# Performance work log

Hardware: AMD Instinct MI355X
Metric: run time of the kernel (lower is better)

Reference implementation:

```python
import jax, jax.numpy as jnp
import numpy as np

B, S, D = 1, 1024, 1024
NH, DH, DR = 8, 128, 64
DCQ, DC = 768, 256
INTER, E, TOPK = 512, 8, 2

def rmsnorm(x, w, eps=1e-6):
    return x * jax.lax.rsqrt(jnp.mean(x * x, -1, keepdims=True) + eps) * w

def lin(x, w, b):
    return x @ w.T + b

def apply_rope(x, cos, sin):
    # x: [b, s, h, d]; cos/sin: [S, d//2]; complex rotate pairs (even, odd)
    b, s, h, d = x.shape
    xr = x.reshape(b, s, h, d // 2, 2)
    x0, x1 = xr[..., 0], xr[..., 1]
    c = cos[None, :s, None, :]
    sn = sin[None, :s, None, :]
    return jnp.stack([x0 * c - x1 * sn, x0 * sn + x1 * c], -1).reshape(b, s, h, d)

def setup_inputs():
    keys = iter(jax.random.split(jax.random.key(0), 64))
    def nrm(*shape):
        return jax.random.normal(next(keys), shape, jnp.float32) * 0.02
    theta = 1.0 / (10000.0 ** (jnp.arange(0, DR, 2, dtype=jnp.float32) / DR))
    ang = jnp.arange(S, dtype=jnp.float32)[:, None] * theta[None, :]
    return dict(
        h=jax.random.normal(next(keys), (B, S, D), jnp.float32),
        freqs_cos=jnp.cos(ang), freqs_sin=jnp.sin(ang),
        mask=jnp.triu(jnp.ones((S, S), bool), 1),
        attn_norm_w=jnp.ones(D), ffn_norm_w=jnp.ones(D),
        wq_down=nrm(DCQ, D), bq_down=jnp.zeros(DCQ), q_norm_w=jnp.ones(DCQ),
        wqc=nrm(NH * DH, DCQ), bqc=jnp.zeros(NH * DH),
        wqr=nrm(NH * DR, DCQ), bqr=jnp.zeros(NH * DR),
        wkr=nrm(DR, D), bkr=jnp.zeros(DR), kr_norm_w=jnp.ones(DR),
        wkv_down=nrm(DC, D), bkv_down=jnp.zeros(DC), kv_norm_w=jnp.ones(DC),
        wkc=nrm(NH * DH, DC), bkc=jnp.zeros(NH * DH),
        wvc=nrm(NH * DH, DC), bvc=jnp.zeros(NH * DH),
        wo=nrm(D, NH * DH), bo=jnp.zeros(D),
        sw1=nrm(INTER, D), sb1=jnp.zeros(INTER), sw2=nrm(D, INTER), sb2=jnp.zeros(D),
        sw3=nrm(INTER, D), sb3=jnp.zeros(INTER),
        ew1=nrm(E, INTER, D), eb1=jnp.zeros((E, INTER)), ew2=nrm(E, D, INTER), eb2=jnp.zeros((E, D)),
        ew3=nrm(E, INTER, D), eb3=jnp.zeros((E, INTER)),
        centroids=jax.random.normal(next(keys), (E, D), jnp.float32), biases=jnp.zeros(E),
    )

def _forward(h, freqs_cos, freqs_sin, mask, attn_norm_w, ffn_norm_w, wq_down, bq_down, q_norm_w, wqc, bqc, wqr, bqr, wkr, bkr, kr_norm_w, wkv_down, bkv_down, kv_norm_w, wkc, bkc, wvc, bvc, wo, bo, sw1, sb1, sw2, sb2, sw3, sb3, ew1, eb1, ew2, eb2, ew3, eb3, centroids, biases):
    b, s, _ = h.shape
    # --- pre-norm MLA attention ---
    x = rmsnorm(h, attn_norm_w)
    cQ = rmsnorm(lin(x, wq_down, bq_down), q_norm_w)
    qR = apply_rope(lin(cQ, wqr, bqr).reshape(b, s, NH, DR), freqs_cos, freqs_sin)
    qC = lin(cQ, wqc, bqc).reshape(b, s, NH, DH)
    q = jnp.concatenate([qC, qR], -1)                      # [b,s,NH,DH+DR]
    kR = apply_rope(rmsnorm(lin(x, wkr, bkr), kr_norm_w).reshape(b, s, 1, DR), freqs_cos, freqs_sin)
    cKV = rmsnorm(lin(x, wkv_down, bkv_down), kv_norm_w)
    kC = lin(cKV, wkc, bkc).reshape(b, s, NH, DH)
    vC = lin(cKV, wvc, bvc).reshape(b, s, NH, DH)
    k = jnp.concatenate([jnp.broadcast_to(kR, (b, s, NH, DR)), kC], -1)  # source order: [kR, kC]
    scores = jnp.einsum('bqhd,bkhd->bhqk', q, k) / jnp.sqrt(jnp.float32(DH + DR))
    scores = jnp.where(mask[None, None], jnp.finfo(scores.dtype).min, scores)
    attw = jax.nn.softmax(scores, -1)                      # dropout in eval mode = identity
    attn = jnp.einsum('bhqk,bkhd->bqhd', attw, vC).reshape(b, s, NH * DH)
    x1 = h + lin(attn, wo, bo)
    # --- pre-norm MoE FFN ---
    y = rmsnorm(x1, ffn_norm_w)
    shared = lin(jax.nn.silu(lin(y, sw1, sb1)) * lin(y, sw3, sb3), sw2, sb2)  # mean over 1 shared expert
    affinity = jax.nn.sigmoid(y @ centroids.T)             # [b,s,E]
    _, topi = jax.lax.top_k(affinity + biases, TOPK)
    gates = jax.nn.softmax(jnp.take_along_axis(affinity, topi, -1), -1)      # [b,s,TOPK]
    combine = (jax.nn.one_hot(topi, E, dtype=y.dtype) * gates[..., None]).sum(-2)  # [b,s,E]
    h1 = jax.nn.silu(jnp.einsum('bsd,eid->bsei', y, ew1) + eb1) * (jnp.einsum('bsd,eid->bsei', y, ew3) + eb3)
    out_e = jnp.einsum('bsei,edi->bsed', h1, ew2) + eb2
    routed = (out_e * combine[..., None]).sum(2)
    return x1 + shared + routed

def reference(h, freqs_cos, freqs_sin, mask, attn_norm_w, ffn_norm_w, wq_down, bq_down, q_norm_w, wqc, bqc, wqr, bqr, wkr, bkr, kr_norm_w, wkv_down, bkv_down, kv_norm_w, wkc, bkc, wvc, bvc, wo, bo, sw1, sb1, sw2, sb2, sw3, sb3, ew1, eb1, ew2, eb2, ew3, eb3, centroids, biases):
    return _forward(h, freqs_cos, freqs_sin, mask, attn_norm_w, ffn_norm_w, wq_down, bq_down, q_norm_w, wqc, bqc, wqr, bqr, wkr, bkr, kr_norm_w, wkv_down, bkv_down, kv_norm_w, wkc, bkc, wvc, bvc, wo, bo, sw1, sb1, sw2, sb2, sw3, sb3, ew1, eb1, ew2, eb2, ew3, eb3, centroids, biases)
```

## Files before the change

### kernel.cpp

```cpp
#include <hip/hip_runtime.h>

typedef unsigned short u16;
typedef __attribute__((ext_vector_type(8))) short short8;
typedef __attribute__((ext_vector_type(4))) float f32x4;

__device__ __forceinline__ float b2f(u16 u) { return __uint_as_float(((unsigned)u) << 16); }
__device__ __forceinline__ u16 f2b(float f) {
    unsigned x = __float_as_uint(f);
    return (u16)((x + 0x7fffu + ((x >> 16) & 1u)) >> 16);
}

#define GLDS16(gp, lp) __builtin_amdgcn_global_load_lds( \
    (const __attribute__((address_space(1))) void*)(gp), \
    (__attribute__((address_space(3))) void*)(lp), 16, 0, 0)

#define WAITV(N) do { \
    asm volatile("s_waitcnt vmcnt(" #N ")" ::: "memory"); \
    __builtin_amdgcn_sched_barrier(0); \
} while (0)

#define KC8_SWZ(lane) ((((lane) & 3) ^ (((lane) >> 3) & 3)) << 3)
#define RD_SWZ(fm, fq) (((fq) ^ (((fm) >> 1) & 3)) << 3)

struct Seg { const u16* W; const float* bias; void* C; int ldc; int epi; int bx0; int aidx; };
struct GArgs {
    const u16* A[2]; int lda[2]; int K[2];
    Seg seg[4]; int nseg;
    const float* res;
    float* dst2;
};

__launch_bounds__(256)
__global__ void mgemm4(GArgs ga)
{
    __shared__ u16 As[4 * 2048];
    __shared__ u16 Bs[4 * 2048];
    int bx = blockIdx.x, by = blockIdx.y;
    int si = 0;
#pragma unroll
    for (int i = 1; i < 4; i++)
        if (i < ga.nseg && bx >= ga.seg[i].bx0) si = i;
    const u16* Wp = ga.seg[si].W;
    const float* bp = ga.seg[si].bias;
    void* Cp = ga.seg[si].C;
    const int ldco = ga.seg[si].ldc;
    const int epi = ga.seg[si].epi;
    const int ai = ga.seg[si].aidx;
    const u16* Ap = ga.A[ai];
    const int lda = ga.lda[ai], K = ga.K[ai];
    const int col0 = (bx - ga.seg[si].bx0) * 64;
    const int row0 = by * 64;

    int tid = threadIdx.x;
    int lane = tid & 63, w = tid >> 6;
    int r0 = (w << 4) + (lane >> 2), kc8 = KC8_SWZ(lane);
    const u16* gA = Ap + (size_t)(row0 + r0) * lda + kc8;
    const u16* gB = Wp + (size_t)(col0 + r0) * lda + kc8;

    int fm = lane & 15, fq = lane >> 4;
    const int so = RD_SWZ(fm, fq);
    f32x4 acc[4] = {};

#define MG_STAGE(BS, KO) do { \
    GLDS16(gA + (KO), As + (BS) * 2048 + (w << 9)); \
    GLDS16(gB + (KO), Bs + (BS) * 2048 + (w << 9)); \
} while (0)

    const int nst = K >> 5;
    MG_STAGE(0, 0);
    MG_STAGE(1, 32);
    MG_STAGE(2, 64);
    int bc = 0;
    for (int t = 0; t < nst; t++) {
        if (t < nst - 2) WAITV(4);
        else if (t == nst - 2) WAITV(2);
        else WAITV(0);
        __builtin_amdgcn_s_barrier();
        if (t + 3 < nst) {
            int bs = bc + 3; if (bs >= 4) bs -= 4;
            MG_STAGE(bs, (t + 3) << 5);
        }
        short8 af = *(const short8*)(As + bc * 2048 + (w << 9) + fm * 32 + so);
        short8 bf[4];
#pragma unroll
        for (int nt = 0; nt < 4; nt++)
            bf[nt] = *(const short8*)(Bs + bc * 2048 + ((nt << 4) + fm) * 32 + so);
#pragma unroll
        for (int nt = 0; nt < 4; nt++)
            acc[nt] = __builtin_amdgcn_mfma_f32_16x16x32_bf16(af, bf[nt], acc[nt], 0, 0, 0);
        bc = (bc + 1) & 3;
    }
#undef MG_STAGE

    int rbase = row0 + (w << 4) + (fq << 2);
#pragma unroll
    for (int nt = 0; nt < 4; nt++) {
        int c = col0 + (nt << 4) + fm;
        float bcol = bp[c];
#pragma unroll
        for (int reg = 0; reg < 4; reg++) {
            int r = rbase + reg;
            float v = acc[nt][reg] + bcol;
            if (epi == 3)
                ((u16*)Cp)[(size_t)r * ldco + c] = f2b(v);
            else if (epi == 1) {
                float o = v + ga.res[(size_t)r * ldco + c];
                ((float*)Cp)[(size_t)r * ldco + c] = o;
                if (ga.dst2) ga.dst2[(size_t)r * ldco + c] = o;
            } else
                ((float*)Cp)[(size_t)r * ldco + c] = v;
        }
    }
}

__launch_bounds__(256)
__global__ void mega_glu(const u16* __restrict__ Y16,
                         const u16* __restrict__ sw1, const float* __restrict__ sb1,
                         const u16* __restrict__ sw3, const float* __restrict__ sb3,
                         const u16* __restrict__ ew1, const float* __restrict__ eb1,
                         const u16* __restrict__ ew3, const float* __restrict__ eb3,
                         u16* __restrict__ Gb,
                         const int* __restrict__ lists, const int* __restrict__ counts)
{
    __shared__ u16 As[4 * 2048];
    __shared__ u16 B1s[4 * 2048];
    __shared__ u16 B3s[4 * 2048];
    int bx = blockIdx.x, by = blockIdx.y, z = blockIdx.z;
    int col0 = bx * 64;
    int cnt = 1024; const int* list = nullptr;
    const u16 *W1p, *W3p; const float *b1p, *b3p;
    if (z == 0) {
        W1p = sw1; b1p = sb1; W3p = sw3; b3p = sb3;
    } else {
        int e = z - 1; cnt = counts[e]; list = lists + (e << 10);
        W1p = ew1 + (size_t)e * 512 * 1024; b1p = eb1 + e * 512;
        W3p = ew3 + (size_t)e * 512 * 1024; b3p = eb3 + e * 512;
    }
    int row0 = by * 64;
    if (row0 >= cnt) return;
    u16* Cp = Gb + (size_t)z * 524288;

    int tid = threadIdx.x, lane = tid & 63, w = tid >> 6;
    int r0 = (w << 4) + (lane >> 2), kc8 = KC8_SWZ(lane);
    int ar = row0 + r0;
    if (z > 0) ar = list[ar < cnt ? ar : cnt - 1];
    const u16* gA = Y16 + (size_t)ar * 1024 + kc8;
    const u16* gB1 = W1p + (size_t)(col0 + r0) * 1024 + kc8;
    const u16* gB3 = W3p + (size_t)(col0 + r0) * 1024 + kc8;

    int fm = lane & 15, fq = lane >> 4;
    const int so = RD_SWZ(fm, fq);
    f32x4 accU[4] = {}, accV[4] = {};

#define GL_STAGE(BS, KO) do { \
    GLDS16(gA + (KO),  As  + (BS) * 2048 + (w << 9)); \
    GLDS16(gB1 + (KO), B1s + (BS) * 2048 + (w << 9)); \
    GLDS16(gB3 + (KO), B3s + (BS) * 2048 + (w << 9)); \
} while (0)

    GL_STAGE(0, 0);
    GL_STAGE(1, 32);
    GL_STAGE(2, 64);
    int bc = 0;
    for (int t = 0; t < 32; t++) {
        if (t < 30) WAITV(6);
        else if (t == 30) WAITV(3);
        else WAITV(0);
        __builtin_amdgcn_s_barrier();
        if (t + 3 < 32) {
            int bs = bc + 3; if (bs >= 4) bs -= 4;
            GL_STAGE(bs, (t + 3) << 5);
        }
        short8 af = *(const short8*)(As + bc * 2048 + (w << 9) + fm * 32 + so);
#pragma unroll
        for (int nt = 0; nt < 4; nt++) {
            short8 b1 = *(const short8*)(B1s + bc * 2048 + ((nt << 4) + fm) * 32 + so);
            accU[nt] = __builtin_amdgcn_mfma_f32_16x16x32_bf16(af, b1, accU[nt], 0, 0, 0);
        }
#pragma unroll
        for (int nt = 0; nt < 4; nt++) {
            short8 b3 = *(const short8*)(B3s + bc * 2048 + ((nt << 4) + fm) * 32 + so);
            accV[nt] = __builtin_amdgcn_mfma_f32_16x16x32_bf16(af, b3, accV[nt], 0, 0, 0);
        }
        bc = (bc + 1) & 3;
    }
#undef GL_STAGE

    int rbase = row0 + (w << 4) + (fq << 2);
#pragma unroll
    for (int nt = 0; nt < 4; nt++) {
        int c = col0 + (nt << 4) + fm;
        float b1c = b1p[c], b3c = b3p[c];
#pragma unroll
        for (int reg = 0; reg < 4; reg++) {
            int r = rbase + reg;
            if (r >= cnt) continue;
            float u = b2f(f2b(accU[nt][reg] + b1c));
            float v = b2f(f2b(accV[nt][reg] + b3c));
            Cp[(size_t)r * 512 + c] = f2b(u / (1.f + __expf(-u)) * v);
        }
    }
}

__launch_bounds__(256)
__global__ void mega_down(const u16* __restrict__ Gb,
                          const u16* __restrict__ sw2, const float* __restrict__ sb2,
                          const u16* __restrict__ ew2, const float* __restrict__ eb2,
                          float* __restrict__ out,
                          const int* __restrict__ lists, const float* __restrict__ glist,
                          const int* __restrict__ counts)
{
    __shared__ u16 Gs[4 * 2048];
    __shared__ u16 Ws[4 * 2048];
    int bx = blockIdx.x, by = blockIdx.y, z = blockIdx.z;
    int cnt = 1024; const int* list = nullptr; const float* gl = nullptr;
    const u16* Wp; const float* bp;
    if (z == 0) { Wp = sw2; bp = sb2; }
    else {
        int e = z - 1;
        cnt = counts[e]; list = lists + (e << 10); gl = glist + (e << 10);
        Wp = ew2 + (size_t)e * 1024 * 512; bp = eb2 + e * 1024;
    }
    int row0 = by * 64;
    if (row0 >= cnt) return;
    const u16* Ap = Gb + (size_t)z * 524288;
    int col0 = bx * 64;

    int tid = threadIdx.x, lane = tid & 63, w = tid >> 6;
    int r0 = (w << 4) + (lane >> 2), kc8 = KC8_SWZ(lane);
    const u16* gG = Ap + (size_t)(row0 + r0) * 512 + kc8;
    const u16* gW = Wp + (size_t)(col0 + r0) * 512 + kc8;

    int fm = lane & 15, fq = lane >> 4;
    const int so = RD_SWZ(fm, fq);
    f32x4 acc[4] = {};

#define MD_STAGE(BS, KO) do { \
    GLDS16(gG + (KO), Gs + (BS) * 2048 + (w << 9)); \
    GLDS16(gW + (KO), Ws + (BS) * 2048 + (w << 9)); \
} while (0)

    MD_STAGE(0, 0);
    MD_STAGE(1, 32);
    MD_STAGE(2, 64);
    int bc = 0;
    for (int t = 0; t < 16; t++) {
        if (t < 14) WAITV(4);
        else if (t == 14) WAITV(2);
        else WAITV(0);
        __builtin_amdgcn_s_barrier();
        if (t + 3 < 16) {
            int bs = bc + 3; if (bs >= 4) bs -= 4;
            MD_STAGE(bs, (t + 3) << 5);
        }
        short8 af = *(const short8*)(Gs + bc * 2048 + (w << 9) + fm * 32 + so);
        short8 bf[4];
#pragma unroll
        for (int nt = 0; nt < 4; nt++)
            bf[nt] = *(const short8*)(Ws + bc * 2048 + ((nt << 4) + fm) * 32 + so);
#pragma unroll
        for (int nt = 0; nt < 4; nt++)
            acc[nt] = __builtin_amdgcn_mfma_f32_16x16x32_bf16(af, bf[nt], acc[nt], 0, 0, 0);
        bc = (bc + 1) & 3;
    }
#undef MD_STAGE

    int rbase = row0 + (w << 4) + (fq << 2);
#pragma unroll
    for (int nt = 0; nt < 4; nt++) {
        int c = col0 + (nt << 4) + fm;
        float bcol = bp[c];
#pragma unroll
        for (int reg = 0; reg < 4; reg++) {
            int r = rbase + reg;
            int tok; float g;
            if (z == 0) { tok = r; g = 1.f; }
            else { if (r >= cnt) continue; tok = list[r]; g = gl[r]; }
            atomicAdd(&out[(size_t)tok * 1024 + c], g * (acc[nt][reg] + bcol));
        }
    }
}

__launch_bounds__(256)
__global__ void attn_mfma(const u16* __restrict__ Qp, const u16* __restrict__ Kp,
                          const u16* __restrict__ VT, u16* __restrict__ O)
{
    const int qt = blockIdx.x, h = blockIdx.y;
    const int q0 = qt * 64;
    const int tid = threadIdx.x;
    const int lane = tid & 63, w = tid >> 6;
    const int fm = lane & 15, fq = lane >> 4;

    __shared__ u16 Ks[2 * 12288];
    __shared__ u16 Vs[4 * 4096];
    __shared__ u16 Ps[4 * 2048];

    const u16* qrow = Qp + ((size_t)h * 1024 + q0 + w * 16 + fm) * 192;
    short8 qf[6];
#pragma unroll
    for (int c = 0; c < 6; c++)
        qf[c] = *(const short8*)(qrow + c * 32 + fq * 8);

    const u16* Kb = Kp + (size_t)h * 1024 * 192;
    const u16* Vb = VT + (size_t)h * 128 * 1024;

    float m_i[4], l_i[4];
#pragma unroll
    for (int r = 0; r < 4; r++) { m_i[r] = -1e30f; l_i[r] = 0.f; }
    f32x4 accO[8] = {};
    const float scale = 0.07216878364870323f;
    const int nkt = (qt >> 1) + 1;
    const int rbase = w * 16 + fq * 4;

    for (int kt = 0; kt < nkt; ++kt) {
        const int kt0 = kt * 128;
#pragma unroll
        for (int half = 0; half < 2; half++) {
            const int o = kt0 + half * 64;
#pragma unroll
            for (int i = 0; i < 6; i++) {
                int idx = w + 4 * i;
                int c = idx >> 2, k4 = idx & 3;
                const u16* g = Kb + (size_t)(o + k4 * 16 + (lane >> 2)) * 192 + c * 32 + (lane & 3) * 8;
                GLDS16(g, Ks + half * 12288 + c * 2048 + k4 * 512 + lane * 8);
            }
#pragma unroll
            for (int i = 0; i < 4; i++) {
                int idx = w + 4 * i;
                int kc = idx >> 3, k8 = idx & 7;
                const u16* g = Vb + (size_t)(k8 * 16 + (lane >> 2)) * 1024 + o + kc * 32 + (lane & 3) * 8;
                GLDS16(g, Vs + (half * 2 + kc) * 4096 + k8 * 512 + lane * 8);
            }
        }
        __syncthreads();
        f32x4 sacc[8];
#pragma unroll
        for (int nt = 0; nt < 8; nt++) {
            sacc[nt] = (f32x4){0.f, 0.f, 0.f, 0.f};
#pragma unroll
            for (int c = 0; c < 6; c++) {
                short8 kf = *(const short8*)(Ks + (nt >> 2) * 12288 + c * 2048 + ((nt & 3) * 16 + fm) * 32 + fq * 8);
                sacc[nt] = __builtin_amdgcn_mfma_f32_16x16x32_bf16(qf[c], kf, sacc[nt], 0, 0, 0);
            }
        }
        float pv[8][4], rmax[4];
#pragma unroll
        for (int reg = 0; reg < 4; reg++) {
            int q = q0 + rbase + reg;
            float mx = -1e30f;
#pragma unroll
            for (int nt = 0; nt < 8; nt++) {
                int gk = kt0 + nt * 16 + fm;
                float s = sacc[nt][reg] * scale;
                if (gk > q) s = -1e30f;
                pv[nt][reg] = s;
                mx = fmaxf(mx, s);
            }
            rmax[reg] = mx;
        }
#pragma unroll
        for (int m = 1; m < 16; m <<= 1)
#pragma unroll
            for (int reg = 0; reg < 4; reg++)
                rmax[reg] = fmaxf(rmax[reg], __shfl_xor(rmax[reg], m));
        float alpha[4], rsum[4];
#pragma unroll
        for (int reg = 0; reg < 4; reg++) {
            float mn = fmaxf(m_i[reg], rmax[reg]);
            alpha[reg] = __expf(m_i[reg] - mn);
            m_i[reg] = mn;
            float s = 0.f;
#pragma unroll
            for (int nt = 0; nt < 8; nt++) {
                float p = __expf(pv[nt][reg] - mn);
                pv[nt][reg] = p;
                s += p;
            }
            rsum[reg] = s;
        }
#pragma unroll
        for (int m = 1; m < 16; m <<= 1)
#pragma unroll
            for (int reg = 0; reg < 4; reg++)
                rsum[reg] += __shfl_xor(rsum[reg], m);
#pragma unroll
        for (int reg = 0; reg < 4; reg++)
            l_i[reg] = l_i[reg] * alpha[reg] + rsum[reg];
#pragma unroll
        for (int nt = 0; nt < 8; nt++)
#pragma unroll
            for (int reg = 0; reg < 4; reg++)
                Ps[w * 2048 + (nt >> 1) * 512 + (fq * 4 + reg) * 32 + (nt & 1) * 16 + fm]
                    = f2b(pv[nt][reg]);
#pragma unroll
        for (int n2 = 0; n2 < 8; n2++)
#pragma unroll
            for (int reg = 0; reg < 4; reg++)
                accO[n2][reg] *= alpha[reg];
        short8 pf[4];
#pragma unroll
        for (int kc = 0; kc < 4; kc++)
            pf[kc] = *(const short8*)(Ps + w * 2048 + kc * 512 + fm * 32 + fq * 8);
#pragma unroll
        for (int n2 = 0; n2 < 8; n2++)
#pragma unroll
            for (int kc = 0; kc < 4; kc++) {
                short8 vf = *(const short8*)(Vs + kc * 4096 + (n2 * 16 + fm) * 32 + fq * 8);
                accO[n2] = __builtin_amdgcn_mfma_f32_16x16x32_bf16(pf[kc], vf, accO[n2], 0, 0, 0);
            }
        __syncthreads();
    }
#pragma unroll
    for (int reg = 0; reg < 4; reg++) {
        int row = q0 + rbase + reg;
        float inv = 1.f / l_i[reg];
#pragma unroll
        for (int n2 = 0; n2 < 8; n2++)
            O[(size_t)row * 1024 + h * 128 + n2 * 16 + fm] = f2b(accO[n2][reg] * inv);
    }
}

__launch_bounds__(256)
__global__ void rmsnorm2x(const float* __restrict__ X0, const float* __restrict__ w0,
                          u16* __restrict__ O0, int c0,
                          const float* __restrict__ X1, const float* __restrict__ w1,
                          u16* __restrict__ O1, int c1)
{
    int b = blockIdx.x, tid = threadIdx.x;
    const float* X; const float* w; u16* O; int cols; int r;
    if (b < 1024) { X = X0; w = w0; O = O0; cols = c0; r = b; }
    else          { X = X1; w = w1; O = O1; cols = c1; r = b - 1024; }
    const float* xr = X + (size_t)r * cols;
    float ss = 0.f;
    for (int j = tid; j < cols; j += 256) { float v = xr[j]; ss += v * v; }
    __shared__ float red[256];
    red[tid] = ss; __syncthreads();
    for (int st = 128; st > 0; st >>= 1) { if (tid < st) red[tid] += red[tid + st]; __syncthreads(); }
    float scale = rsqrtf(red[0] / cols + 1e-6f);
    for (int j = tid; j < cols; j += 256)
        O[(size_t)r * cols + j] = f2b(xr[j] * scale * w[j]);
}

__launch_bounds__(256)
__global__ void rmsnorm_route(const float* __restrict__ X1, const float* __restrict__ ffnw,
                              u16* __restrict__ Y16,
                              const float* __restrict__ cent, const float* __restrict__ biases,
                              int* __restrict__ counts, int* __restrict__ lists,
                              float* __restrict__ glist)
{
    __shared__ float red[256];
    int b = blockIdx.x, tid = threadIdx.x;
    if (b < 1024) {
        int r = b;
        const float* xr = X1 + (size_t)r * 1024;
        float ss = 0.f;
        for (int j = tid; j < 1024; j += 256) { float v = xr[j]; ss += v * v; }
        red[tid] = ss; __syncthreads();
        for (int st = 128; st > 0; st >>= 1) { if (tid < st) red[tid] += red[tid + st]; __syncthreads(); }
        float scale = rsqrtf(red[0] / 1024.f + 1e-6f);
        for (int j = tid; j < 1024; j += 256)
            Y16[(size_t)r * 1024 + j] = f2b(xr[j] * scale * ffnw[j]);
    } else {
        int t = b - 1024;
        const float* xr = X1 + (size_t)t * 1024;
        float ss = 0.f;
        float acc[8] = {};
        for (int j = tid; j < 1024; j += 256) {
            float x = xr[j];
            ss += x * x;
            float yp = x * ffnw[j];
#pragma unroll
            for (int e = 0; e < 8; e++) acc[e] += yp * cent[e * 1024 + j];
        }
        red[tid] = ss; __syncthreads();
        for (int st = 128; st > 0; st >>= 1) { if (tid < st) red[tid] += red[tid + st]; __syncthreads(); }
        float scale = rsqrtf(red[0] / 1024.f + 1e-6f);
        __syncthreads();
        __shared__ float aff[8];
        for (int e = 0; e < 8; e++) {
            red[tid] = acc[e]; __syncthreads();
            for (int st = 128; st > 0; st >>= 1) { if (tid < st) red[tid] += red[tid + st]; __syncthreads(); }
            if (tid == 0) aff[e] = 1.f / (1.f + expf(-red[0] * scale));
            __syncthreads();
        }
        if (tid == 0) {
            float sb[8];
#pragma unroll
            for (int e = 0; e < 8; e++) sb[e] = aff[e] + biases[e];
            int i0 = 0;
            for (int e = 1; e < 8; e++) if (sb[e] > sb[i0]) i0 = e;
            int i1 = -1;
            for (int e = 0; e < 8; e++) { if (e == i0) continue; if (i1 < 0 || sb[e] > sb[i1]) i1 = e; }
            float a0 = aff[i0], a1 = aff[i1];
            float mx = fmaxf(a0, a1);
            float e0 = expf(a0 - mx), e1 = expf(a1 - mx);
            float inv = 1.f / (e0 + e1);
            int p0 = atomicAdd(&counts[i0], 1);
            lists[i0 * 1024 + p0] = t; glist[i0 * 1024 + p0] = e0 * inv;
            int p1 = atomicAdd(&counts[i1], 1);
            lists[i1 * 1024 + p1] = t; glist[i1 * 1024 + p1] = e1 * inv;
        }
    }
}

__launch_bounds__(256)
__global__ void pack_all(const float* __restrict__ QC, const float* __restrict__ QRr,
                         const float* __restrict__ KRraw, const float* __restrict__ krw,
                         const float* __restrict__ KC,
                         const u16* __restrict__ VCb,
                         const float* __restrict__ fcos, const float* __restrict__ fsin,
                         u16* __restrict__ Qp, u16* __restrict__ Kp, u16* __restrict__ VT)
{
    __shared__ u16 Ts[64][68];
    __shared__ float kshared[64];
    int b = blockIdx.x, tid = threadIdx.x;
    if (b < 1024) {
        int s = b;
        if (tid < 64) {
            float v = KRraw[(size_t)s * 64 + tid];
            float ss = v * v;
#pragma unroll
            for (int m = 1; m < 64; m <<= 1) ss += __shfl_xor(ss, m);
            float scale = rsqrtf(ss / 64.f + 1e-6f);
            int j = tid >> 1;
            float c = fcos[s * 32 + j], sn = fsin[s * 32 + j];
            float x0 = KRraw[(size_t)s * 64 + (tid & ~1)] * scale * krw[tid & ~1];
            float x1 = KRraw[(size_t)s * 64 + (tid | 1)]  * scale * krw[tid | 1];
            kshared[tid] = (tid & 1) ? (x0 * sn + x1 * c) : (x0 * c - x1 * sn);
        }
        __syncthreads();
        for (int e = tid; e < 1536; e += 256) {
            int h = e / 192, d = e % 192;
            float q;
            if (d < 128) {
                q = QC[(size_t)s * 1024 + h * 128 + d];
            } else {
                int dd = d - 128, j = dd >> 1;
                float c = fcos[s * 32 + j], sn = fsin[s * 32 + j];
                float x0 = QRr[(size_t)s * 512 + h * 64 + (dd & ~1)];
                float x1 = QRr[(size_t)s * 512 + h * 64 + (dd | 1)];
                q = (dd & 1) ? (x0 * sn + x1 * c) : (x0 * c - x1 * sn);
            }
            Qp[((size_t)h * 1024 + s) * 192 + d] = f2b(q);
            float k = (d < 64) ? kshared[d]
                               : KC[(size_t)s * 1024 + h * 128 + d - 64];
            Kp[((size_t)h * 1024 + s) * 192 + d] = f2b(k);
        }
    } else {
        int idx = b - 1024;
        int s0 = (idx & 15) * 64, d0 = (idx >> 4) * 64;
        for (int k = 0; k < 16; k++) {
            int e = tid + k * 256, r = e >> 6, c = e & 63;
            Ts[r][c] = VCb[(size_t)(s0 + r) * 1024 + d0 + c];
        }
        __syncthreads();
        for (int k = 0; k < 16; k++) {
            int e = tid + k * 256, d = e >> 6, s = e & 63;
            VT[(size_t)(d0 + d) * 1024 + s0 + s] = Ts[s][d];
        }
    }
}

#define NCAST 4096
__launch_bounds__(256)
__global__ void fused_cast(const float* p0, const float* p1, const float* p2,
                           const float* p3, const float* p4, const float* p5,
                           const float* p6, const float* p7, const float* p8,
                           const float* p9, const float* p10, const float* p11,
                           const float* p12, const float* pkr,
                           u16* __restrict__ dst,
                           const float* __restrict__ hX, const float* __restrict__ attnw,
                           u16* __restrict__ X16)
{
    __shared__ float red[256];
    int b = blockIdx.x, tid = threadIdx.x;
    if (b < NCAST) {
        const int NQ = 18022400 / 4;
        for (int i = b * 256 + tid; i < NQ; i += NCAST * 256) {
            int e = i * 4;
            const float* s; int base;
            if      (e <   786432) { s = p0;  base = 0; }
            else if (e <  1048576) { s = p1;  base =   786432; }
            else if (e <  1835008) { s = p2;  base =  1048576; }
            else if (e <  2228224) { s = p3;  base =  1835008; }
            else if (e <  2490368) { s = p4;  base =  2228224; }
            else if (e <  2752512) { s = p5;  base =  2490368; }
            else if (e <  3801088) { s = p6;  base =  2752512; }
            else if (e <  4325376) { s = p7;  base =  3801088; }
            else if (e <  4849664) { s = p8;  base =  4325376; }
            else if (e <  5373952) { s = p9;  base =  4849664; }
            else if (e <  9568256) { s = p10; base =  5373952; }
            else if (e < 13762560) { s = p11; base =  9568256; }
            else if (e < 17956864) { s = p12; base = 13762560; }
            else                   { s = pkr; base = 17956864; }
            float4 v = *(const float4*)(s + (e - base));
            ushort4 o;
            o.x = f2b(v.x); o.y = f2b(v.y); o.z = f2b(v.z); o.w = f2b(v.w);
            *(ushort4*)(dst + e) = o;
        }
    } else {
        int r = b - NCAST;
        const float* xr = hX + (size_t)r * 1024;
        float ss = 0.f;
        for (int j = tid; j < 1024; j += 256) { float v = xr[j]; ss += v * v; }
        red[tid] = ss; __syncthreads();
        for (int st = 128; st > 0; st >>= 1) { if (tid < st) red[tid] += red[tid + st]; __syncthreads(); }
        float scale = rsqrtf(red[0] / 1024.f + 1e-6f);
        for (int j = tid; j < 1024; j += 256)
            X16[(size_t)r * 1024 + j] = f2b(xr[j] * scale * attnw[j]);
    }
}

extern "C" void kernel_launch(void* const* d_in, const int* in_sizes, int n_in,
                              void* d_out, int out_size, void* d_ws, size_t ws_size,
                              hipStream_t stream)
{
    (void)in_sizes; (void)n_in; (void)ws_size; (void)out_size;
    const float* h       = (const float*)d_in[0];
    const float* fcos    = (const float*)d_in[1];
    const float* fsin    = (const float*)d_in[2];
    const float* attn_w  = (const float*)d_in[4];
    const float* ffn_w   = (const float*)d_in[5];
    const float* wq_down = (const float*)d_in[6];
    const float* bq_down = (const float*)d_in[7];
    const float* q_norm  = (const float*)d_in[8];
    const float* wqc     = (const float*)d_in[9];
    const float* bqc     = (const float*)d_in[10];
    const float* wqr     = (const float*)d_in[11];
    const float* bqr     = (const float*)d_in[12];
    const float* wkr     = (const float*)d_in[13];
    const float* bkr     = (const float*)d_in[14];
    const float* kr_norm = (const float*)d_in[15];
    const float* wkv     = (const float*)d_in[16];
    const float* bkv     = (const float*)d_in[17];
    const float* kv_norm = (const float*)d_in[18];
    const float* wkc     = (const float*)d_in[19];
    const float* bkc     = (const float*)d_in[20];
    const float* wvc     = (const float*)d_in[21];
    const float* bvc     = (const float*)d_in[22];
    const float* wo      = (const float*)d_in[23];
    const float* bo      = (const float*)d_in[24];
    const float* sw1     = (const float*)d_in[25];
    const float* sb1     = (const float*)d_in[26];
    const float* sw2     = (const float*)d_in[27];
    const float* sb2     = (const float*)d_in[28];
    const float* sw3     = (const float*)d_in[29];
    const float* sb3     = (const float*)d_in[30];
    const float* ew1     = (const float*)d_in[31];
    const float* eb1     = (const float*)d_in[32];
    const float* ew2     = (const float*)d_in[33];
    const float* eb2     = (const float*)d_in[34];
    const float* ew3     = (const float*)d_in[35];
    const float* eb3     = (const float*)d_in[36];
    const float* cent    = (const float*)d_in[37];
    const float* biases  = (const float*)d_in[38];

    char* wsb = (char*)d_ws;
    const size_t U5 = 512 * 1024;
    u16*   X16   = (u16*)(wsb + 8 * U5);
    float* QRr   = (float*)(wsb + 12 * U5);
    float* CQraw = (float*)(wsb + 16 * U5);
    u16*   ATT16 = (u16*)(wsb + 16 * U5);
    u16*   CQ16  = (u16*)(wsb + 22 * U5);
    float* CKVraw= (float*)(wsb + 25 * U5);
    u16*   CKV16 = (u16*)(wsb + 27 * U5);
    float* KRraw = (float*)(wsb + 28 * U5);
    float* QC    = (float*)(wsb + 29 * U5);
    float* KC    = (float*)(wsb + 37 * U5);
    float* X1    = (float*)(wsb + 53 * U5);
    float* GL    = (float*)(wsb + 61 * U5);
    int*   lists = (int*)(wsb + 61 * U5 + 32 * 1024);
    int*   counts= (int*)(wsb + 61 * U5 + 64 * 1024);
    u16*   Y16   = (u16*)(wsb + 69 * U5);
    u16*   Gb    = (u16*)(wsb + 73 * U5);

    u16* wb = (u16*)(wsb + 92 * U5);
    u16 *c_wq  = wb;
    u16 *c_wkv = c_wq  + 786432;
    u16 *c_wqc = c_wkv + 262144;
    u16 *c_wqr = c_wqc + 786432;
    u16 *c_wkc = c_wqr + 393216;
    u16 *c_wvc = c_wkc + 262144;
    u16 *c_wo  = c_wvc + 262144;
    u16 *c_sw1 = c_wo  + 1048576;
    u16 *c_sw3 = c_sw1 + 524288;
    u16 *c_sw2 = c_sw3 + 524288;
    u16 *c_ew1 = c_sw2 + 524288;
    u16 *c_ew3 = c_ew1 + 4194304;
    u16 *c_ew2 = c_ew3 + 4194304;
    u16 *c_wkr = c_ew2 + 4194304;
    u16* VCb = (u16*)(wsb + 92 * U5 + 36175872);
    u16* VTp = VCb + 1048576;
    u16* Qpk = VTp + 1048576;
    u16* Kpk = Qpk + 1572864;

    fused_cast<<<NCAST + 1024, 256, 0, stream>>>(wq_down, wkv, wqc, wqr, wkc, wvc, wo,
                                                 sw1, sw3, sw2, ew1, ew3, ew2, wkr, wb,
                                                 h, attn_w, X16);

    {
        GArgs g = {};
        g.A[0] = X16; g.lda[0] = 1024; g.K[0] = 1024;
        g.seg[0] = { c_wq,  bq_down, CQraw,  768, 0, 0,  0 };
        g.seg[1] = { c_wkv, bkv,     CKVraw, 256, 0, 12, 0 };
        g.seg[2] = { c_wkr, bkr,     KRraw,  64,  0, 16, 0 };
        g.nseg = 3;
        mgemm4<<<dim3(17, 16), 256, 0, stream>>>(g);
    }
    rmsnorm2x<<<2048, 256, 0, stream>>>(CQraw, q_norm, CQ16, 768,
                                        CKVraw, kv_norm, CKV16, 256);
    {
        GArgs g = {};
        g.A[0] = CQ16;  g.lda[0] = 768; g.K[0] = 768;
        g.A[1] = CKV16; g.lda[1] = 256; g.K[1] = 256;
        g.seg[0] = { c_wqc, bqc, QC,   1024, 0, 0,  0 };
        g.seg[1] = { c_wqr, bqr, QRr,  512,  0, 16, 0 };
        g.seg[2] = { c_wkc, bkc, KC,   1024, 0, 24, 1 };
        g.seg[3] = { c_wvc, bvc, VCb,  1024, 3, 40, 1 };
        g.nseg = 4;
        mgemm4<<<dim3(56, 16), 256, 0, stream>>>(g);
    }
    pack_all<<<1280, 256, 0, stream>>>(QC, QRr, KRraw, kr_norm, KC, VCb, fcos, fsin,
                                       Qpk, Kpk, VTp);
    attn_mfma<<<dim3(16, 8), 256, 0, stream>>>(Qpk, Kpk, VTp, ATT16);
    {
        GArgs g = {};
        g.A[0] = ATT16; g.lda[0] = 1024; g.K[0] = 1024;
        g.seg[0] = { c_wo, bo, X1, 1024, 1, 0, 0 };
        g.nseg = 1; g.res = h; g.dst2 = (float*)d_out;
        mgemm4<<<dim3(16, 16), 256, 0, stream>>>(g);
    }

    hipMemsetAsync(counts, 0, 32, stream);
    rmsnorm_route<<<2048, 256, 0, stream>>>(X1, ffn_w, Y16, cent, biases,
                                            counts, lists, GL);
    mega_glu<<<dim3(8, 16, 9), 256, 0, stream>>>(Y16, c_sw1, sb1, c_sw3, sb3,
                                                 c_ew1, eb1, c_ew3, eb3,
                                                 Gb, lists, counts);
    mega_down<<<dim3(16, 16, 9), 256, 0, stream>>>(Gb, c_sw2, sb2, c_ew2, eb2,
                                                   (float*)d_out, lists, GL, counts);
}
```

Before: 370.5 us.

## Split attention over KV halves with combine kernel, deepen GEMM pipelines

The attention kernel now splits each query tile's causal KV range into two halves across a new grid z dimension. Each half writes unnormalised partial outputs and its running max and sum, and a new combine kernel merges them. This doubles the block count from 128, which underfills the GPU, and adds s_setprio around the MFMA sections. Separately, all three GEMM kernels move from a 4-stage to a 6-stage LDS ring that processes two k-steps per barrier. The costs are more LDS per block, an extra launch, and fp32 partial-output traffic.

```diff
diff --git a/kernel.cpp b/kernel.cpp
--- a/kernel.cpp
+++ b/kernel.cpp
@@ -33,8 +33,8 @@
 __launch_bounds__(256)
 __global__ void mgemm4(GArgs ga)
 {
-    __shared__ u16 As[4 * 2048];
-    __shared__ u16 Bs[4 * 2048];
+    __shared__ u16 As[6 * 2048];
+    __shared__ u16 Bs[6 * 2048];
     int bx = blockIdx.x, by = blockIdx.y;
     int si = 0;
 #pragma unroll
@@ -67,28 +67,28 @@
 } while (0)
 
     const int nst = K >> 5;
-    MG_STAGE(0, 0);
-    MG_STAGE(1, 32);
-    MG_STAGE(2, 64);
-    int bc = 0;
-    for (int t = 0; t < nst; t++) {
-        if (t < nst - 2) WAITV(4);
-        else if (t == nst - 2) WAITV(2);
-        else WAITV(0);
+    MG_STAGE(0, 0); MG_STAGE(1, 32); MG_STAGE(2, 64); MG_STAGE(3, 96);
+    int bcur = 0;
+    for (int t = 0; t < nst; t += 2) {
+        if (t < nst - 2) { WAITV(4); } else { WAITV(0); }
         __builtin_amdgcn_s_barrier();
-        if (t + 3 < nst) {
-            int bs = bc + 3; if (bs >= 4) bs -= 4;
-            MG_STAGE(bs, (t + 3) << 5);
-        }
-        short8 af = *(const short8*)(As + bc * 2048 + (w << 9) + fm * 32 + so);
-        short8 bf[4];
-#pragma unroll
-        for (int nt = 0; nt < 4; nt++)
-            bf[nt] = *(const short8*)(Bs + bc * 2048 + ((nt << 4) + fm) * 32 + so);
-#pragma unroll
-        for (int nt = 0; nt < 4; nt++)
-            acc[nt] = __builtin_amdgcn_mfma_f32_16x16x32_bf16(af, bf[nt], acc[nt], 0, 0, 0);
-        bc = (bc + 1) & 3;
+        int w4 = bcur + 4; if (w4 >= 6) w4 -= 6;
+        int w5 = w4 + 1;   if (w5 >= 6) w5 -= 6;
+        if (t + 4 < nst) MG_STAGE(w4, (t + 4) << 5);
+        if (t + 5 < nst) MG_STAGE(w5, (t + 5) << 5);
+#pragma unroll
+        for (int sub = 0; sub < 2; sub++) {
+            int bc = bcur + sub; if (bc >= 6) bc -= 6;
+            short8 af = *(const short8*)(As + bc * 2048 + (w << 9) + fm * 32 + so);
+            short8 bf[4];
+#pragma unroll
+            for (int nt = 0; nt < 4; nt++)
+                bf[nt] = *(const short8*)(Bs + bc * 2048 + ((nt << 4) + fm) * 32 + so);
+#pragma unroll
+            for (int nt = 0; nt < 4; nt++)
+                acc[nt] = __builtin_amdgcn_mfma_f32_16x16x32_bf16(af, bf[nt], acc[nt], 0, 0, 0);
+        }
+        bcur += 2; if (bcur >= 6) bcur -= 6;
     }
 #undef MG_STAGE
 
@@ -122,9 +122,9 @@
                          u16* __restrict__ Gb,
                          const int* __restrict__ lists, const int* __restrict__ counts)
 {
-    __shared__ u16 As[4 * 2048];
-    __shared__ u16 B1s[4 * 2048];
-    __shared__ u16 B3s[4 * 2048];
+    __shared__ u16 As[6 * 2048];
+    __shared__ u16 B1s[6 * 2048];
+    __shared__ u16 B3s[6 * 2048];
     int bx = blockIdx.x, by = blockIdx.y, z = blockIdx.z;
     int col0 = bx * 64;
     int cnt = 1024; const int* list = nullptr;
@@ -158,31 +158,31 @@
     GLDS16(gB3 + (KO), B3s + (BS) * 2048 + (w << 9)); \
 } while (0)
 
-    GL_STAGE(0, 0);
-    GL_STAGE(1, 32);
-    GL_STAGE(2, 64);
-    int bc = 0;
-    for (int t = 0; t < 32; t++) {
-        if (t < 30) WAITV(6);
-        else if (t == 30) WAITV(3);
-        else WAITV(0);
+    GL_STAGE(0, 0); GL_STAGE(1, 32); GL_STAGE(2, 64); GL_STAGE(3, 96);
+    int bcur = 0;
+    for (int t = 0; t < 32; t += 2) {
+        if (t < 30) { WAITV(6); } else { WAITV(0); }
         __builtin_amdgcn_s_barrier();
-        if (t + 3 < 32) {
-            int bs = bc + 3; if (bs >= 4) bs -= 4;
-            GL_STAGE(bs, (t + 3) << 5);
-        }
-        short8 af = *(const short8*)(As + bc * 2048 + (w << 9) + fm * 32 + so);
-#pragma unroll
-        for (int nt = 0; nt < 4; nt++) {
-            short8 b1 = *(const short8*)(B1s + bc * 2048 + ((nt << 4) + fm) * 32 + so);
-            accU[nt] = __builtin_amdgcn_mfma_f32_16x16x32_bf16(af, b1, accU[nt], 0, 0, 0);
-        }
-#pragma unroll
-        for (int nt = 0; nt < 4; nt++) {
-            short8 b3 = *(const short8*)(B3s + bc * 2048 + ((nt << 4) + fm) * 32 + so);
-            accV[nt] = __builtin_amdgcn_mfma_f32_16x16x32_bf16(af, b3, accV[nt], 0, 0, 0);
-        }
-        bc = (bc + 1) & 3;
+        int w4 = bcur + 4; if (w4 >= 6) w4 -= 6;
+        int w5 = w4 + 1;   if (w5 >= 6) w5 -= 6;
+        if (t + 4 < 32) GL_STAGE(w4, (t + 4) << 5);
+        if (t + 5 < 32) GL_STAGE(w5, (t + 5) << 5);
+#pragma unroll
+        for (int sub = 0; sub < 2; sub++) {
+            int bc = bcur + sub; if (bc >= 6) bc -= 6;
+            short8 af = *(const short8*)(As + bc * 2048 + (w << 9) + fm * 32 + so);
+#pragma unroll
+            for (int nt = 0; nt < 4; nt++) {
+                short8 b1 = *(const short8*)(B1s + bc * 2048 + ((nt << 4) + fm) * 32 + so);
+                accU[nt] = __builtin_amdgcn_mfma_f32_16x16x32_bf16(af, b1, accU[nt], 0, 0, 0);
+            }
+#pragma unroll
+            for (int nt = 0; nt < 4; nt++) {
+                short8 b3 = *(const short8*)(B3s + bc * 2048 + ((nt << 4) + fm) * 32 + so);
+                accV[nt] = __builtin_amdgcn_mfma_f32_16x16x32_bf16(af, b3, accV[nt], 0, 0, 0);
+            }
+        }
+        bcur += 2; if (bcur >= 6) bcur -= 6;
     }
 #undef GL_STAGE
 
@@ -210,8 +210,8 @@
                           const int* __restrict__ lists, const float* __restrict__ glist,
                           const int* __restrict__ counts)
 {
-    __shared__ u16 Gs[4 * 2048];
-    __shared__ u16 Ws[4 * 2048];
+    __shared__ u16 Gs[6 * 2048];
+    __shared__ u16 Ws[6 * 2048];
     int bx = blockIdx.x, by = blockIdx.y, z = blockIdx.z;
     int cnt = 1024; const int* list = nullptr; const float* gl = nullptr;
     const u16* Wp; const float* bp;
@@ -240,28 +240,28 @@
     GLDS16(gW + (KO), Ws + (BS) * 2048 + (w << 9)); \
 } while (0)
 
-    MD_STAGE(0, 0);
-    MD_STAGE(1, 32);
-    MD_STAGE(2, 64);
-    int bc = 0;
-    for (int t = 0; t < 16; t++) {
-        if (t < 14) WAITV(4);
-        else if (t == 14) WAITV(2);
-        else WAITV(0);
+    MD_STAGE(0, 0); MD_STAGE(1, 32); MD_STAGE(2, 64); MD_STAGE(3, 96);
+    int bcur = 0;
+    for (int t = 0; t < 16; t += 2) {
+        if (t < 14) { WAITV(4); } else { WAITV(0); }
         __builtin_amdgcn_s_barrier();
-        if (t + 3 < 16) {
-            int bs = bc + 3; if (bs >= 4) bs -= 4;
-            MD_STAGE(bs, (t + 3) << 5);
-        }
-        short8 af = *(const short8*)(Gs + bc * 2048 + (w << 9) + fm * 32 + so);
-        short8 bf[4];
-#pragma unroll
-        for (int nt = 0; nt < 4; nt++)
-            bf[nt] = *(const short8*)(Ws + bc * 2048 + ((nt << 4) + fm) * 32 + so);
-#pragma unroll
-        for (int nt = 0; nt < 4; nt++)
-            acc[nt] = __builtin_amdgcn_mfma_f32_16x16x32_bf16(af, bf[nt], acc[nt], 0, 0, 0);
-        bc = (bc + 1) & 3;
+        int w4 = bcur + 4; if (w4 >= 6) w4 -= 6;
+        int w5 = w4 + 1;   if (w5 >= 6) w5 -= 6;
+        if (t + 4 < 16) MD_STAGE(w4, (t + 4) << 5);
+        if (t + 5 < 16) MD_STAGE(w5, (t + 5) << 5);
+#pragma unroll
+        for (int sub = 0; sub < 2; sub++) {
+            int bc = bcur + sub; if (bc >= 6) bc -= 6;
+            short8 af = *(const short8*)(Gs + bc * 2048 + (w << 9) + fm * 32 + so);
+            short8 bf[4];
+#pragma unroll
+            for (int nt = 0; nt < 4; nt++)
+                bf[nt] = *(const short8*)(Ws + bc * 2048 + ((nt << 4) + fm) * 32 + so);
+#pragma unroll
+            for (int nt = 0; nt < 4; nt++)
+                acc[nt] = __builtin_amdgcn_mfma_f32_16x16x32_bf16(af, bf[nt], acc[nt], 0, 0, 0);
+        }
+        bcur += 2; if (bcur >= 6) bcur -= 6;
     }
 #undef MD_STAGE
 
@@ -283,9 +283,10 @@
 
 __launch_bounds__(256)
 __global__ void attn_mfma(const u16* __restrict__ Qp, const u16* __restrict__ Kp,
-                          const u16* __restrict__ VT, u16* __restrict__ O)
-{
-    const int qt = blockIdx.x, h = blockIdx.y;
+                          const u16* __restrict__ VT,
+                          float* __restrict__ Opart, float* __restrict__ MLp)
+{
+    const int qt = blockIdx.x, h = blockIdx.y, z = blockIdx.z;
     const int q0 = qt * 64;
     const int tid = threadIdx.x;
     const int lane = tid & 63, w = tid >> 6;
@@ -310,9 +311,12 @@
     f32x4 accO[8] = {};
     const float scale = 0.07216878364870323f;
     const int nkt = (qt >> 1) + 1;
+    const int half0 = (nkt + 1) >> 1;
+    const int ktlo = z ? half0 : 0;
+    const int kthi = z ? nkt : half0;
     const int rbase = w * 16 + fq * 4;
 
-    for (int kt = 0; kt < nkt; ++kt) {
+    for (int kt = ktlo; kt < kthi; ++kt) {
         const int kt0 = kt * 128;
 #pragma unroll
         for (int half = 0; half < 2; half++) {
@@ -334,6 +338,7 @@
         }
         __syncthreads();
         f32x4 sacc[8];
+        __builtin_amdgcn_s_setprio(1);
 #pragma unroll
         for (int nt = 0; nt < 8; nt++) {
             sacc[nt] = (f32x4){0.f, 0.f, 0.f, 0.f};
@@ -343,6 +348,7 @@
                 sacc[nt] = __builtin_amdgcn_mfma_f32_16x16x32_bf16(qf[c], kf, sacc[nt], 0, 0, 0);
             }
         }
+        __builtin_amdgcn_s_setprio(0);
         float pv[8][4], rmax[4];
 #pragma unroll
         for (int reg = 0; reg < 4; reg++) {
@@ -401,6 +407,7 @@
 #pragma unroll
         for (int kc = 0; kc < 4; kc++)
             pf[kc] = *(const short8*)(Ps + w * 2048 + kc * 512 + fm * 32 + fq * 8);
+        __builtin_amdgcn_s_setprio(1);
 #pragma unroll
         for (int n2 = 0; n2 < 8; n2++)
 #pragma unroll
@@ -408,15 +415,45 @@
                 short8 vf = *(const short8*)(Vs + kc * 4096 + (n2 * 16 + fm) * 32 + fq * 8);
                 accO[n2] = __builtin_amdgcn_mfma_f32_16x16x32_bf16(pf[kc], vf, accO[n2], 0, 0, 0);
             }
+        __builtin_amdgcn_s_setprio(0);
         __syncthreads();
     }
+    float* Ob = Opart + ((size_t)(z * 8 + h) * 1024) * 128;
 #pragma unroll
     for (int reg = 0; reg < 4; reg++) {
         int row = q0 + rbase + reg;
-        float inv = 1.f / l_i[reg];
 #pragma unroll
         for (int n2 = 0; n2 < 8; n2++)
-            O[(size_t)row * 1024 + h * 128 + n2 * 16 + fm] = f2b(accO[n2][reg] * inv);
+            Ob[(size_t)row * 128 + n2 * 16 + fm] = accO[n2][reg];
+        if (fm == 0) {
+            MLp[((size_t)(z * 8 + h) * 1024 + row) * 2]     = m_i[reg];
+            MLp[((size_t)(z * 8 + h) * 1024 + row) * 2 + 1] = l_i[reg];
+        }
+    }
+}
+
+__launch_bounds__(256)
+__global__ void attn_combine(const float* __restrict__ Opart,
+                             const float* __restrict__ MLp,
+                             u16* __restrict__ O)
+{
+    int tid = threadIdx.x;
+    int rowg = blockIdx.x * 16 + (tid >> 4);
+    int h = rowg >> 10, row = rowg & 1023;
+    int c0 = (tid & 15) * 8;
+    const float* O0 = Opart + ((size_t)h * 1024 + row) * 128;
+    const float* O1 = Opart + ((size_t)(8 + h) * 1024 + row) * 128;
+    float m0 = MLp[((size_t)h * 1024 + row) * 2];
+    float l0 = MLp[((size_t)h * 1024 + row) * 2 + 1];
+    float m1 = MLp[((size_t)(8 + h) * 1024 + row) * 2];
+    float l1 = MLp[((size_t)(8 + h) * 1024 + row) * 2 + 1];
+    float M = fmaxf(m0, m1);
+    float w0 = __expf(m0 - M), w1 = __expf(m1 - M);
+    float inv = 1.f / (l0 * w0 + l1 * w1);
+#pragma unroll
+    for (int j = 0; j < 8; j++) {
+        float o = (O0[c0 + j] * w0 + O1[c0 + j] * w1) * inv;
+        O[(size_t)row * 1024 + h * 128 + c0 + j] = f2b(o);
     }
 }
 
@@ -693,6 +730,8 @@
     u16* VTp = VCb + 1048576;
     u16* Qpk = VTp + 1048576;
     u16* Kpk = Qpk + 1572864;
+    float* Opart = (float*)(wsb + 192 * U5);
+    float* MLp   = (float*)(wsb + 209 * U5);
 
     fused_cast<<<NCAST + 1024, 256, 0, stream>>>(wq_down, wkv, wqc, wqr, wkc, wvc, wo,
                                                  sw1, sw3, sw2, ew1, ew3, ew2, wkr, wb,
@@ -722,7 +761,8 @@
     }
     pack_all<<<1280, 256, 0, stream>>>(QC, QRr, KRraw, kr_norm, KC, VCb, fcos, fsin,
                                        Qpk, Kpk, VTp);
-    attn_mfma<<<dim3(16, 8), 256, 0, stream>>>(Qpk, Kpk, VTp, ATT16);
+    attn_mfma<<<dim3(16, 8, 2), 256, 0, stream>>>(Qpk, Kpk, VTp, Opart, MLp);
+    attn_combine<<<512, 256, 0, stream>>>(Opart, MLp, ATT16);
     {
         GArgs g = {};
         g.A[0] = ATT16; g.lda[0] = 1024; g.K[0] = 1024;
```

Result: faster. 354.8 us (-4.2%).
